# Performance work log

Measured on AMD Instinct MI355X. Metric: run time of the kernel, lower is better.

## Reference

```python
import jax, jax.numpy as jnp
import numpy as np

D_K = 766  # feature dim, also softmax temperature per module init
NEG = -1000000000.0


def setup_inputs() -> dict:
    key = jax.random.key(0)
    k1, k2, k3 = jax.random.split(key, 3)
    B, H, L, D = 2, 4, 2048, D_K
    Q = jax.random.normal(k1, (B, H, L, D), dtype=jnp.float32)
    K = jax.random.normal(k2, (B, H, L, D), dtype=jnp.float32)
    attn_mask = jax.random.randint(k3, (B, H, L, L), 0, 2) > 0  # bool [B,H,Lk,Lq]
    return {"Q": Q, "K": K, "attn_mask": attn_mask}


def reference(Q, K, attn_mask):
    # scores: [B,H,Lq,Lk]
    scores = jnp.einsum("bhqd,bhkd->bhqk", Q, K) / np.sqrt(D_K).astype(np.float32)
    # mask is [B,H,Lk,Lq]; torch applies mask.transpose(2,3)
    scores = jnp.where(jnp.swapaxes(attn_mask, 2, 3), NEG, scores)
    attn1 = jax.nn.softmax(scores, axis=-1)                       # row softmax
    attn2 = jax.nn.softmax(jnp.swapaxes(scores, -1, -2), axis=-1)  # col softmax
    # dropout prob = 0.0 -> identity
    context1 = jnp.einsum("bhqk,bhkd->bhqd", attn1, K)
    context2 = jnp.einsum("bhkq,bhqd->bhkd", attn2, Q)
    return (context1, context2, attn1, attn2)
```

## Files before the change

kernel.cpp:

```cpp
#include <hip/hip_runtime.h>
#include <math.h>

#define L 2048
#define DK 766
#define DKP 768
#define NBH 8
#define NR (NBH * L)
#define NEGV -1000000000.0f

typedef __attribute__((ext_vector_type(8))) short bf16x8_t;
typedef __attribute__((ext_vector_type(4))) float f32x4_t;

#define LDT 72

typedef __attribute__((address_space(1))) const unsigned int gu32;
typedef __attribute__((address_space(3))) unsigned int lu32;

__device__ __forceinline__ short f2bf(float x) {
    union { float f; unsigned u; } v;
    v.f = x;
    unsigned r = v.u + 0x7fff + ((v.u >> 16) & 1);
    return (short)(r >> 16);
}

__device__ __forceinline__ float bf2f(short s) {
    union { unsigned u; float f; } v;
    v.u = ((unsigned)(unsigned short)s) << 16;
    return v.f;
}

__device__ __forceinline__ void gl_lds16(const void* g, void* l) {
    __builtin_amdgcn_global_load_lds((gu32*)g, (lu32*)l, 16, 0, 0);
}

#define BARR() asm volatile("s_barrier" ::: "memory")
#define VMW() asm volatile("s_waitcnt vmcnt(0)" ::: "memory")
#define PRIO1() __builtin_amdgcn_s_setprio(1)
#define PRIO0() __builtin_amdgcn_s_setprio(0)

__global__ __launch_bounds__(256) void k_cvtT(const float* __restrict__ Q,
                                              const float* __restrict__ K,
                                              short* __restrict__ Qb,
                                              short* __restrict__ Kb,
                                              short* __restrict__ Qt,
                                              short* __restrict__ Kt) {
    __shared__ short T[64 * LDT];
    const int tz = blockIdx.z;
    const int bh = tz & 7;
    const float* X = (tz < 8) ? Q : K;
    short* Xb = (tz < 8) ? Qb : Kb;
    short* Xt = (tz < 8) ? Qt : Kt;
    X += (size_t)bh * L * DK;
    Xb += (size_t)bh * L * DKP;
    Xt += (size_t)bh * DKP * L;
    const int r0 = blockIdx.y * 64, c0 = blockIdx.x * 64;
    const int t = threadIdx.x;
    const int rl = t >> 2, cc = (t & 3) * 16;

    bf16x8_t v0, v1;
#pragma unroll
    for (int p = 0; p < 8; ++p) {
        int c = c0 + cc + 2 * p;
        float2 f = (c < DK) ? *(const float2*)&X[(size_t)(r0 + rl) * DK + c]
                            : make_float2(0.f, 0.f);
        if (p < 4) { v0[2 * p] = f2bf(f.x); v0[2 * p + 1] = f2bf(f.y); }
        else { v1[2 * (p - 4)] = f2bf(f.x); v1[2 * (p - 4) + 1] = f2bf(f.y); }
    }
    *(bf16x8_t*)&Xb[(size_t)(r0 + rl) * DKP + c0 + cc] = v0;
    *(bf16x8_t*)&Xb[(size_t)(r0 + rl) * DKP + c0 + cc + 8] = v1;
    *(bf16x8_t*)&T[rl * LDT + cc] = v0;
    *(bf16x8_t*)&T[rl * LDT + cc + 8] = v1;
    __syncthreads();
    bf16x8_t w0, w1;
#pragma unroll
    for (int p = 0; p < 8; ++p) {
        w0[p] = T[(cc + p) * LDT + rl];
        w1[p] = T[(cc + 8 + p) * LDT + rl];
    }
    *(bf16x8_t*)&Xt[(size_t)(c0 + rl) * L + r0 + cc] = w0;
    *(bf16x8_t*)&Xt[(size_t)(c0 + rl) * L + r0 + cc + 8] = w1;
}

__global__ __launch_bounds__(512, 4) void k_score2(const short* __restrict__ Kb,
                                                   const short* __restrict__ Qb,
                                                   const int* __restrict__ mask,
                                                   short* __restrict__ Sb,
                                                   float* __restrict__ prowM,
                                                   float* __restrict__ prowS,
                                                   float* __restrict__ pcolM,
                                                   float* __restrict__ pcolS) {
    __shared__ __align__(16) short LB[24576];

    int flat = blockIdx.x;
    int nw = (flat & 7) * 128 + (flat >> 3);
    int bh = nw >> 7, rem = nw & 127;
    int byp = rem >> 4, bxp = rem & 15;
    const short* Am = Kb + (size_t)bh * L * DKP;
    const short* Bm = Qb + (size_t)bh * L * DKP;
    const int* Mm = mask + (size_t)bh * L * L;
    short* Sm = Sb + (size_t)bh * L * L;
    const int m0 = byp * 256, n0 = bxp * 128;

    const int t = threadIdx.x, lane = t & 63, wid = t >> 6;
    const int wr = wid >> 1, wc = wid & 1;
    const int lr = lane & 15, lg = lane >> 4;

    const int schunk = (lane & 7) ^ (lane >> 3);
    const short* aSrc = Am + (size_t)(m0 + wid * 32 + (lane >> 3)) * DKP + schunk * 8;
    const short* bSrc = Bm + (size_t)(n0 + wid * 16 + (lane >> 3)) * DKP + schunk * 8;
    char* ldsA = (char*)LB;
    char* ldsB = (char*)LB + 32768;

    const int axr = lr & 7;
    const int kc0 = ((0 + lg) ^ axr) * 8;
    const int kc1 = ((4 + lg) ^ axr) * 8;

    f32x4_t acc[4][4];
#pragma unroll
    for (int i = 0; i < 4; ++i)
#pragma unroll
        for (int j = 0; j < 4; ++j) acc[i][j] = f32x4_t{0.f, 0.f, 0.f, 0.f};

    const int NT = DKP / 64;
    for (int kt = 0; kt < NT; ++kt) {
        const int k0 = kt * 64;
#pragma unroll
        for (int g = 0; g < 4; ++g)
            gl_lds16(aSrc + (size_t)(8 * g) * DKP + k0, ldsA + wid * 4096 + g * 1024);
#pragma unroll
        for (int g = 0; g < 2; ++g)
            gl_lds16(bSrc + (size_t)(8 * g) * DKP + k0, ldsB + wid * 2048 + g * 1024);
        VMW();
        BARR();
        PRIO1();
#pragma unroll
        for (int ks = 0; ks < 2; ++ks) {
            const int kc = ks ? kc1 : kc0;
            bf16x8_t av[4], bv[4];
#pragma unroll
            for (int i = 0; i < 4; ++i)
                av[i] = *(const bf16x8_t*)&LB[wr * 4096 + i * 1024 + lr * 64 + kc];
#pragma unroll
            for (int j = 0; j < 4; ++j)
                bv[j] = *(const bf16x8_t*)&LB[16384 + wc * 4096 + j * 1024 + lr * 64 + kc];
#pragma unroll
            for (int i = 0; i < 4; ++i)
#pragma unroll
                for (int j = 0; j < 4; ++j)
                    acc[i][j] = __builtin_amdgcn_mfma_f32_16x16x32_bf16(
                        av[i], bv[j], acc[i][j], 0, 0, 0);
        }
        PRIO0();
        BARR();
    }

    const float scale = 1.0f / sqrtf((float)DK);
#pragma unroll
    for (int i = 0; i < 4; ++i) {
        int krow = m0 + wr * 64 + i * 16 + lg * 4;
#pragma unroll
        for (int j = 0; j < 4; ++j) {
            int qcol = n0 + wc * 64 + j * 16 + lr;
#pragma unroll
            for (int r = 0; r < 4; ++r) {
                int mv = Mm[(size_t)(krow + r) * L + qcol];
                float v = mv ? NEGV : acc[i][j][r] * scale;
                acc[i][j][r] = v;
                Sm[(size_t)(krow + r) * L + qcol] = f2bf(v);
            }
        }
    }

    __syncthreads();
    float* redb = (float*)LB;

#pragma unroll
    for (int i = 0; i < 4; ++i) {
#pragma unroll
        for (int r = 0; r < 4; ++r) {
            float rm = fmaxf(fmaxf(acc[i][0][r], acc[i][1][r]),
                             fmaxf(acc[i][2][r], acc[i][3][r]));
#pragma unroll
            for (int m = 1; m < 16; m <<= 1) rm = fmaxf(rm, __shfl_xor(rm, m, 64));
            float rs = 0.f;
#pragma unroll
            for (int j = 0; j < 4; ++j) rs += expf(acc[i][j][r] - rm);
#pragma unroll
            for (int m = 1; m < 16; m <<= 1) rs += __shfl_xor(rs, m, 64);
            if (lr == 0) {
                int kr = wr * 64 + i * 16 + lg * 4 + r;
                redb[wc * 256 + kr] = rm;
                redb[512 + wc * 256 + kr] = rs;
            }
        }
    }
#pragma unroll
    for (int j = 0; j < 4; ++j) {
        float cm = -INFINITY;
#pragma unroll
        for (int i = 0; i < 4; ++i)
#pragma unroll
            for (int r = 0; r < 4; ++r) cm = fmaxf(cm, acc[i][j][r]);
        cm = fmaxf(cm, __shfl_xor(cm, 16, 64));
        cm = fmaxf(cm, __shfl_xor(cm, 32, 64));
        float cs = 0.f;
#pragma unroll
        for (int i = 0; i < 4; ++i)
#pragma unroll
            for (int r = 0; r < 4; ++r) cs += expf(acc[i][j][r] - cm);
        cs += __shfl_xor(cs, 16, 64);
        cs += __shfl_xor(cs, 32, 64);
        if (lg == 0) {
            int qc = wc * 64 + j * 16 + lr;
            redb[1024 + wr * 128 + qc] = cm;
            redb[1536 + wr * 128 + qc] = cs;
        }
    }
    __syncthreads();
    if (t < 256) {
        float mA = redb[t], mB = redb[256 + t];
        float sA = redb[512 + t], sB = redb[512 + 256 + t];
        float m = fmaxf(mA, mB);
        float s = sA * expf(mA - m) + sB * expf(mB - m);
        size_t o = (size_t)bxp * NR + bh * L + m0 + t;
        prowM[o] = m;
        prowS[o] = s;
    } else if (t < 384) {
        int qc = t - 256;
        float m = redb[1024 + qc];
#pragma unroll
        for (int w = 1; w < 4; ++w) m = fmaxf(m, redb[1024 + w * 128 + qc]);
        float s = 0.f;
#pragma unroll
        for (int w = 0; w < 4; ++w)
            s += redb[1536 + w * 128 + qc] * expf(redb[1024 + w * 128 + qc] - m);
        size_t o = (size_t)byp * NR + bh * L + n0 + qc;
        pcolM[o] = m;
        pcolS[o] = s;
    }
}

__global__ __launch_bounds__(256) void k_comb(const float* __restrict__ prowM,
                                              const float* __restrict__ prowS,
                                              const float* __restrict__ pcolM,
                                              const float* __restrict__ pcolS,
                                              float* __restrict__ m1,
                                              float* __restrict__ r1,
                                              float* __restrict__ m2,
                                              float* __restrict__ r2) {
    int idx = blockIdx.x * 256 + threadIdx.x;
    float m = -INFINITY;
#pragma unroll
    for (int c = 0; c < 16; ++c) m = fmaxf(m, prowM[(size_t)c * NR + idx]);
    float s = 0.f;
#pragma unroll
    for (int c = 0; c < 16; ++c)
        s += prowS[(size_t)c * NR + idx] * expf(prowM[(size_t)c * NR + idx] - m);
    m2[idx] = m;
    r2[idx] = 1.0f / s;

    m = -INFINITY;
#pragma unroll
    for (int c = 0; c < 8; ++c) m = fmaxf(m, pcolM[(size_t)c * NR + idx]);
    s = 0.f;
#pragma unroll
    for (int c = 0; c < 8; ++c)
        s += pcolS[(size_t)c * NR + idx] * expf(pcolM[(size_t)c * NR + idx] - m);
    m1[idx] = m;
    r1[idx] = 1.0f / s;
}

__global__ __launch_bounds__(256) void k_apply(const short* __restrict__ Sb,
                                               const float* __restrict__ mr,
                                               const float* __restrict__ rr,
                                               const float* __restrict__ mc,
                                               const float* __restrict__ rc,
                                               float* __restrict__ OutIn,
                                               float* __restrict__ OutTr,
                                               short* __restrict__ bIn,
                                               short* __restrict__ bTr) {
    __shared__ float T[64][65];
    const int bh = blockIdx.z;
    const int rb0 = blockIdx.x * 64, cb0 = blockIdx.y * 64;
    const short* Sm = Sb + (size_t)bh * L * L;
    float* Oin = OutIn + (size_t)bh * L * L;
    float* Otr = OutTr + (size_t)bh * L * L;
    const int t = threadIdx.x, tx = t & 15, ty = t >> 4;

    float4 mcv = *(const float4*)&mc[bh * L + cb0 + tx * 4];
    float4 rcv = *(const float4*)&rc[bh * L + cb0 + tx * 4];

#pragma unroll
    for (int i = 0; i < 4; ++i) {
        int r = rb0 + ty * 4 + i;
        float mrv = mr[bh * L + r], rrv = rr[bh * L + r];
        short4 sx = *(const short4*)&Sm[(size_t)r * L + cb0 + tx * 4];
        float x0 = bf2f(sx.x), x1 = bf2f(sx.y), x2 = bf2f(sx.z), x3 = bf2f(sx.w);
        float4 e = make_float4(expf(x0 - mrv) * rrv, expf(x1 - mrv) * rrv,
                               expf(x2 - mrv) * rrv, expf(x3 - mrv) * rrv);
        *(float4*)&Oin[(size_t)r * L + cb0 + tx * 4] = e;
        short4 b = make_short4(f2bf(e.x), f2bf(e.y), f2bf(e.z), f2bf(e.w));
        *(short4*)&bIn[(size_t)bh * L * L + (size_t)r * L + cb0 + tx * 4] = b;
        T[tx * 4 + 0][ty * 4 + i] = expf(x0 - mcv.x) * rcv.x;
        T[tx * 4 + 1][ty * 4 + i] = expf(x1 - mcv.y) * rcv.y;
        T[tx * 4 + 2][ty * 4 + i] = expf(x2 - mcv.z) * rcv.z;
        T[tx * 4 + 3][ty * 4 + i] = expf(x3 - mcv.w) * rcv.w;
    }
    __syncthreads();
#pragma unroll
    for (int i = 0; i < 4; ++i) {
        int c = ty * 4 + i;
        float4 v = make_float4(T[c][tx * 4], T[c][tx * 4 + 1], T[c][tx * 4 + 2],
                               T[c][tx * 4 + 3]);
        *(float4*)&Otr[(size_t)(cb0 + c) * L + rb0 + tx * 4] = v;
        short4 b = make_short4(f2bf(v.x), f2bf(v.y), f2bf(v.z), f2bf(v.w));
        *(short4*)&bTr[(size_t)bh * L * L + (size_t)(cb0 + c) * L + rb0 + tx * 4] = b;
    }
}

__global__ __launch_bounds__(512, 2) void k_ctx8(const short* __restrict__ a1b,
                                                 const short* __restrict__ a2b,
                                                 const short* __restrict__ Kt,
                                                 const short* __restrict__ Qt,
                                                 float* __restrict__ c1,
                                                 float* __restrict__ c2) {
    __shared__ __align__(16) short LB[57344];

    int flat = blockIdx.x;
    int nw = (flat & 7) * 64 + (flat >> 3);
    int inst = nw >> 5, rem = nw & 31;
    int myp = rem >> 2, nxp = rem & 3;
    int bh = inst & 7;
    const short* Am = ((inst < 8) ? a1b : a2b) + (size_t)bh * L * L;
    const short* Bt = ((inst < 8) ? Kt : Qt) + (size_t)bh * DKP * L;
    float* Cm = ((inst < 8) ? c1 : c2) + (size_t)bh * L * DK;
    const int m0 = myp * 256, n0 = nxp * 192;

    const int t = threadIdx.x, lane = t & 63, wid = t >> 6;
    const int wr = wid >> 2, wc = wid & 3;
    const int lr = lane & 15, lg = lane >> 4;

    const int schunk = (lane & 7) ^ (lane >> 3);
    const short* aSrc = Am + (size_t)(m0 + wid * 8 + (lane >> 3)) * L + schunk * 8;
    const short* bSrc = Bt + (size_t)(n0 + wid * 8 + (lane >> 3)) * L + schunk * 8;
    char* ldsA = (char*)LB;
    char* ldsB = (char*)LB + 65536;

#define STAGEA(cb, k0n)                                                               \
    do {                                                                              \
        gl_lds16(aSrc + (k0n), ldsA + (cb)*32768 + wid * 1024);                       \
        gl_lds16(aSrc + (size_t)64 * L + (k0n), ldsA + (cb)*32768 + 8192 + wid * 1024); \
        gl_lds16(aSrc + (size_t)128 * L + (k0n), ldsA + (cb)*32768 + 16384 + wid * 1024); \
        gl_lds16(aSrc + (size_t)192 * L + (k0n), ldsA + (cb)*32768 + 24576 + wid * 1024); \
    } while (0)
#define STAGEB(cb, k0n)                                                               \
    do {                                                                              \
        gl_lds16(bSrc + (k0n), ldsB + (cb)*24576 + wid * 1024);                       \
        gl_lds16(bSrc + (size_t)64 * L + (k0n), ldsB + (cb)*24576 + 8192 + wid * 1024); \
        gl_lds16(bSrc + (size_t)128 * L + (k0n), ldsB + (cb)*24576 + 16384 + wid * 1024); \
    } while (0)

    const int axr = lr & 7;
    const int kc0 = ((0 + lg) ^ axr) * 8;
    const int kc1 = ((4 + lg) ^ axr) * 8;
    const int aRd = wr * 8192 + lr * 64;
    const int bRd = 32768 + (wc * 48 + lr) * 64;

#define LDA0(c, i) (*(const bf16x8_t*)&LB[(c)*16384 + aRd + (i)*1024 + kc0])
#define LDA1(c, i) (*(const bf16x8_t*)&LB[(c)*16384 + aRd + (i)*1024 + kc1])
#define LDB0(c, j) (*(const bf16x8_t*)&LB[bRd + (c)*12288 + (j)*1024 + kc0])
#define LDB1(c, j) (*(const bf16x8_t*)&LB[bRd + (c)*12288 + (j)*1024 + kc1])

    f32x4_t acc[8][3];
#pragma unroll
    for (int i = 0; i < 8; ++i)
#pragma unroll
        for (int j = 0; j < 3; ++j) acc[i][j] = f32x4_t{0.f, 0.f, 0.f, 0.f};

    bf16x8_t bfr[3][2];

#define PHASE(c, i0, EXTRA)                                                           \
    do {                                                                              \
        bf16x8_t a00 = LDA0(c, i0), a01 = LDA1(c, i0);                                \
        bf16x8_t a10 = LDA0(c, (i0) + 1), a11 = LDA1(c, (i0) + 1);                    \
        EXTRA;                                                                        \
        BARR();                                                                       \
        PRIO1();                                                                      \
        _Pragma("unroll") for (int j = 0; j < 3; ++j) {                               \
            acc[i0][j] = __builtin_amdgcn_mfma_f32_16x16x32_bf16(a00, bfr[j][0],      \
                                                                 acc[i0][j], 0, 0, 0); \
            acc[i0][j] = __builtin_amdgcn_mfma_f32_16x16x32_bf16(a01, bfr[j][1],      \
                                                                 acc[i0][j], 0, 0, 0); \
            acc[(i0) + 1][j] = __builtin_amdgcn_mfma_f32_16x16x32_bf16(               \
                a10, bfr[j][0], acc[(i0) + 1][j], 0, 0, 0);                           \
            acc[(i0) + 1][j] = __builtin_amdgcn_mfma_f32_16x16x32_bf16(               \
                a11, bfr[j][1], acc[(i0) + 1][j], 0, 0, 0);                           \
        }                                                                             \
        PRIO0();                                                                      \
    } while (0)

    const int NT = L / 64;
    STAGEA(0, 0);
    STAGEB(0, 0);
    VMW();
    BARR();

    for (int kt = 0; kt < NT; ++kt) {
        const int c = kt & 1;
        const bool ds = (kt + 1 < NT);
        const int k0n = (kt + 1) * 64;
#pragma unroll
        for (int j = 0; j < 3; ++j) {
            bfr[j][0] = LDB0(c, j);
            bfr[j][1] = LDB1(c, j);
        }
        PHASE(c, 0, if (ds) STAGEA(c ^ 1, k0n));
        BARR();
        PHASE(c, 2, if (ds) STAGEB(c ^ 1, k0n));
        BARR();
        PHASE(c, 4, ((void)0));
        BARR();
        PHASE(c, 6, ((void)0));
        if (ds) VMW();
        BARR();
    }

#pragma unroll
    for (int i = 0; i < 8; ++i) {
        int row = m0 + wr * 128 + i * 16 + lg * 4;
#pragma unroll
        for (int j = 0; j < 3; ++j) {
            int col = n0 + wc * 48 + j * 16 + lr;
            if (col < DK) {
#pragma unroll
                for (int r = 0; r < 4; ++r)
                    Cm[(size_t)(row + r) * DK + col] = acc[i][j][r];
            }
        }
    }
#undef PHASE
#undef STAGEA
#undef STAGEB
#undef LDA0
#undef LDA1
#undef LDB0
#undef LDB1
}

extern "C" void kernel_launch(void* const* d_in, const int* in_sizes, int n_in,
                              void* d_out, int out_size, void* d_ws, size_t ws_size,
                              hipStream_t stream) {
    const float* Q = (const float*)d_in[0];
    const float* K = (const float*)d_in[1];
    const int* mask = (const int*)d_in[2];
    float* out = (float*)d_out;

    const size_t CTX = (size_t)NBH * L * DK;
    const size_t ATT = (size_t)NBH * L * L;
    float* c1 = out;
    float* c2 = out + CTX;
    float* a1 = out + 2 * CTX;
    float* a2 = out + 2 * CTX + ATT;

    float* ws = (float*)d_ws;
    float* m1 = ws;
    float* r1 = ws + NR;
    float* m2 = ws + 2 * (size_t)NR;
    float* r2 = ws + 3 * (size_t)NR;
    const size_t QBE = (size_t)NBH * L * DKP;
    short* Qb = (short*)(ws + 4 * (size_t)NR);
    short* Kb = Qb + QBE;
    short* a1b = Kb + QBE;
    short* a2b = a1b + ATT;
    short* Qt = a2b + ATT;
    short* Kt = Qt + QBE;

    float* prowM = c1;
    float* prowS = c1 + 16 * (size_t)NR;
    float* pcolM = c1 + 32 * (size_t)NR;
    float* pcolS = c1 + 40 * (size_t)NR;

    dim3 blk(256);

    k_cvtT<<<dim3(12, 32, 16), blk, 0, stream>>>(Q, K, Qb, Kb, Qt, Kt);
    k_score2<<<dim3(1024), dim3(512), 0, stream>>>(Kb, Qb, mask, a2b, prowM, prowS,
                                                   pcolM, pcolS);
    k_comb<<<dim3(NR / 256), blk, 0, stream>>>(prowM, prowS, pcolM, pcolS, m1, r1,
                                               m2, r2);
    k_apply<<<dim3(32, 32, NBH), blk, 0, stream>>>(a2b, m2, r2, m1, r1, a2, a1, a2b,
                                                   a1b);
    k_ctx8<<<dim3(512), dim3(512), 0, stream>>>(a1b, a2b, Kt, Qt, c1, c2);
}
```

Baseline: 411.2 us.

## Overlap next K-tile global-to-LDS loads with second half of MFMA compute

```diff
diff --git a/kernel.cpp b/kernel.cpp
--- a/kernel.cpp
+++ b/kernel.cpp
@@ -35,6 +35,7 @@
 
 #define BARR() asm volatile("s_barrier" ::: "memory")
 #define VMW() asm volatile("s_waitcnt vmcnt(0)" ::: "memory")
+#define LKW() asm volatile("s_waitcnt lgkmcnt(0)" ::: "memory")
 #define PRIO1() __builtin_amdgcn_s_setprio(1)
 #define PRIO0() __builtin_amdgcn_s_setprio(0)
 
@@ -122,36 +123,64 @@
         for (int j = 0; j < 4; ++j) acc[i][j] = f32x4_t{0.f, 0.f, 0.f, 0.f};
 
     const int NT = DKP / 64;
+
+#pragma unroll
+    for (int g = 0; g < 4; ++g)
+        gl_lds16(aSrc + (size_t)(8 * g) * DKP, ldsA + wid * 4096 + g * 1024);
+#pragma unroll
+    for (int g = 0; g < 2; ++g)
+        gl_lds16(bSrc + (size_t)(8 * g) * DKP, ldsB + wid * 2048 + g * 1024);
+
     for (int kt = 0; kt < NT; ++kt) {
-        const int k0 = kt * 64;
-#pragma unroll
-        for (int g = 0; g < 4; ++g)
-            gl_lds16(aSrc + (size_t)(8 * g) * DKP + k0, ldsA + wid * 4096 + g * 1024);
-#pragma unroll
-        for (int g = 0; g < 2; ++g)
-            gl_lds16(bSrc + (size_t)(8 * g) * DKP + k0, ldsB + wid * 2048 + g * 1024);
         VMW();
         BARR();
-        PRIO1();
-#pragma unroll
-        for (int ks = 0; ks < 2; ++ks) {
-            const int kc = ks ? kc1 : kc0;
+        {
             bf16x8_t av[4], bv[4];
 #pragma unroll
             for (int i = 0; i < 4; ++i)
-                av[i] = *(const bf16x8_t*)&LB[wr * 4096 + i * 1024 + lr * 64 + kc];
+                av[i] = *(const bf16x8_t*)&LB[wr * 4096 + i * 1024 + lr * 64 + kc0];
 #pragma unroll
             for (int j = 0; j < 4; ++j)
-                bv[j] = *(const bf16x8_t*)&LB[16384 + wc * 4096 + j * 1024 + lr * 64 + kc];
+                bv[j] =
+                    *(const bf16x8_t*)&LB[16384 + wc * 4096 + j * 1024 + lr * 64 + kc0];
+            PRIO1();
 #pragma unroll
             for (int i = 0; i < 4; ++i)
 #pragma unroll
                 for (int j = 0; j < 4; ++j)
                     acc[i][j] = __builtin_amdgcn_mfma_f32_16x16x32_bf16(
                         av[i], bv[j], acc[i][j], 0, 0, 0);
-        }
+            PRIO0();
+        }
+        bf16x8_t av1[4], bv1[4];
+#pragma unroll
+        for (int i = 0; i < 4; ++i)
+            av1[i] = *(const bf16x8_t*)&LB[wr * 4096 + i * 1024 + lr * 64 + kc1];
+#pragma unroll
+        for (int j = 0; j < 4; ++j)
+            bv1[j] = *(const bf16x8_t*)&LB[16384 + wc * 4096 + j * 1024 + lr * 64 + kc1];
+        LKW();
+        BARR();
+        if (kt + 1 < NT) {
+            const int k0n = (kt + 1) * 64;
+#pragma unroll
+            for (int g = 0; g < 4; ++g)
+                gl_lds16(aSrc + (size_t)(8 * g) * DKP + k0n,
+                         ldsA + wid * 4096 + g * 1024);
+#pragma unroll
+            for (int g = 0; g < 2; ++g)
+                gl_lds16(bSrc + (size_t)(8 * g) * DKP + k0n,
+                         ldsB + wid * 2048 + g * 1024);
+            __builtin_amdgcn_sched_barrier(0);
+        }
+        PRIO1();
+#pragma unroll
+        for (int i = 0; i < 4; ++i)
+#pragma unroll
+            for (int j = 0; j < 4; ++j)
+                acc[i][j] = __builtin_amdgcn_mfma_f32_16x16x32_bf16(
+                    av1[i], bv1[j], acc[i][j], 0, 0, 0);
         PRIO0();
-        BARR();
     }
 
     const float scale = 1.0f / sqrtf((float)DK);
```

New measurement: 414.2 us. About the same (+0.7%).
